# Performance work log

Hardware: AMD Instinct MI355X
Metric: run time of the kernel (lower is better)

## Reference

```python
import jax, jax.numpy as jnp
import numpy as np

STRIDE, PAD, DIL, DG, K = 1, 1, 1, 1, 3


def _conv2d(x, w, b, stride, pad):
    out = jax.lax.conv_general_dilated(
        x, w, (stride, stride), [(pad, pad), (pad, pad)],
        dimension_numbers=("NCHW", "OIHW", "NCHW"))
    return out + b[None, :, None, None]


def _deform_conv(x, weight, bias, offset, mask):
    # x: [B,C,H,W]; offset: [B, 2*DG*K*K, Ho, Wo] (y,x interleaved per tap);
    # mask: [B, DG*K*K, Ho, Wo]; weight: [Cout, C, K, K]
    B, C, H, W = x.shape
    Cout = weight.shape[0]
    KK = K * K
    Ho, Wo = offset.shape[2], offset.shape[3]
    Cg = C // DG

    off = offset.reshape(B, DG, KK, 2, Ho, Wo)
    dy, dx = off[:, :, :, 0], off[:, :, :, 1]          # [B,DG,KK,Ho,Wo]

    ky = (jnp.arange(KK) // K).astype(jnp.float32) * DIL
    kx = (jnp.arange(KK) % K).astype(jnp.float32) * DIL
    oy = (jnp.arange(Ho).astype(jnp.float32) * STRIDE - PAD)
    ox = (jnp.arange(Wo).astype(jnp.float32) * STRIDE - PAD)
    py = dy + ky[None, None, :, None, None] + oy[None, None, None, :, None]
    px = dx + kx[None, None, :, None, None] + ox[None, None, None, None, :]

    y0 = jnp.floor(py)
    x0 = jnp.floor(px)
    wy = py - y0
    wx = px - x0
    y0i = y0.astype(jnp.int32)
    x0i = x0.astype(jnp.int32)

    x_g = x.reshape(B, DG, Cg, H * W)
    val = jnp.zeros((B, DG, Cg, KK, Ho, Wo), dtype=x.dtype)
    corners = [(y0i, x0i, (1 - wy) * (1 - wx)),
               (y0i, x0i + 1, (1 - wy) * wx),
               (y0i + 1, x0i, wy * (1 - wx)),
               (y0i + 1, x0i + 1, wy * wx)]
    for iy, ix, wgt in corners:
        valid = ((iy >= 0) & (iy < H) & (ix >= 0) & (ix < W)).astype(x.dtype)
        idx = jnp.clip(iy, 0, H - 1) * W + jnp.clip(ix, 0, W - 1)  # [B,DG,KK,Ho,Wo]
        g = jnp.take_along_axis(x_g, idx.reshape(B, DG, 1, KK * Ho * Wo), axis=3)
        g = g.reshape(B, DG, Cg, KK, Ho, Wo)
        val = val + g * (wgt * valid)[:, :, None]

    m = mask.reshape(B, DG, 1, KK, Ho, Wo)
    val = (val * m).reshape(B, C, KK, Ho, Wo)
    out = jnp.einsum("bckhw,ock->bohw", val, weight.reshape(Cout, C, KK))
    return out + bias[None, :, None, None]


def setup_inputs() -> dict:
    key = jax.random.key(0)
    ks = jax.random.split(key, 5)
    B, C, H, W, Cout = 8, 64, 128, 128, 64
    x = jax.random.normal(ks[0], (B, C, H, W), dtype=jnp.float32)
    stdv = 1.0 / np.sqrt(C * K * K)
    weight = jax.random.uniform(ks[1], (Cout, C, K, K), minval=-stdv, maxval=stdv, dtype=jnp.float32)
    bias = jnp.zeros((Cout,), dtype=jnp.float32)
    # conv_offset params are zero-init in the original; use small random values
    offset_w = jax.random.normal(ks[2], (3 * DG * K * K, C, K, K), dtype=jnp.float32) * 0.01
    offset_b = jax.random.normal(ks[3], (3 * DG * K * K,), dtype=jnp.float32) * 0.01
    return {"x": x, "weight": weight, "bias": bias, "offset_w": offset_w, "offset_b": offset_b}


def reference(x, weight, bias, offset_w, offset_b):
    split = 2 * DG * K * K
    out = _conv2d(x, offset_w, offset_b, STRIDE, PAD)
    offset = out[:, :split]
    mask = jax.nn.sigmoid(out[:, split:])
    return _deform_conv(x, weight, bias, offset, mask)
```

## Files before the change

kernel.cpp:

```cpp
#include <hip/hip_runtime.h>
#include <hip/hip_bf16.h>
#include <math.h>

#define HH 128
#define WW 128
#define HW 16384
#define BATCH 8

#define TR 8
#define TC 16
#define HALO 2
#define PR 12
#define PC 20
#define PST 36

typedef __attribute__((ext_vector_type(8))) short short8;
typedef __attribute__((ext_vector_type(16))) float f32x16;
typedef __attribute__((ext_vector_type(4))) unsigned int u32x4;

union FragU { short8 v; unsigned int u[4]; u32x4 q; };

static __device__ __forceinline__ unsigned short f2bf(float f) {
    __hip_bfloat16 h = __float2bfloat16(f);
    return *(unsigned short*)&h;
}
static __device__ __forceinline__ float bf_lo(unsigned int r) {
    return __uint_as_float(r << 16);
}
static __device__ __forceinline__ float bf_hi(unsigned int r) {
    return __uint_as_float(r & 0xffff0000u);
}
static __device__ __forceinline__ short8 bilerp_frag(
    u32x4 r00, u32x4 r01, u32x4 r10, u32x4 r11,
    float w0, float w1, float w2, float w3)
{
    FragU bf;
#pragma unroll
    for (int d = 0; d < 4; ++d) {
        float se = fmaf(bf_lo(r11[d]), w3, fmaf(bf_lo(r10[d]), w2,
                   fmaf(bf_lo(r01[d]), w1, bf_lo(r00[d]) * w0)));
        float so = fmaf(bf_hi(r11[d]), w3, fmaf(bf_hi(r10[d]), w2,
                   fmaf(bf_hi(r01[d]), w1, bf_hi(r00[d]) * w0)));
        float2 f2; f2.x = se; f2.y = so;
        __hip_bfloat162 h2 = __float22bfloat162_rn(f2);
        bf.u[d] = *(unsigned int*)&h2;
    }
    return bf.v;
}

__global__ __launch_bounds__(256) void prep_kernel(
    const float* __restrict__ weight,
    const float* __restrict__ offset_w,
    unsigned short* __restrict__ wA,
    unsigned short* __restrict__ owA)
{
    int id = blockIdx.x * 256 + threadIdx.x;
    if (id < 4608) {
        int m = id / 2304;
        int rem = id % 2304;
        int kk = rem >> 8;
        int s = (rem >> 6) & 3;
        int l = id & 63;
        int cout = m * 32 + (l & 31);
        int cbase = s * 16 + 8 * (l >> 5);
#pragma unroll
        for (int j = 0; j < 8; ++j) {
            wA[id * 8 + j] = f2bf(weight[(cout * 64 + cbase + j) * 9 + kk]);
        }
        return;
    }
    int id2 = id - 4608;
    if (id2 < 2304) {
        int kk = id2 >> 8;
        int s = (id2 >> 6) & 3;
        int l = id2 & 63;
        int cout = l & 31;
        int cbase = s * 16 + 8 * (l >> 5);
#pragma unroll
        for (int j = 0; j < 8; ++j) {
            float v = (cout < 27) ? offset_w[(cout * 64 + cbase + j) * 9 + kk] : 0.0f;
            owA[id2 * 8 + j] = f2bf(v);
        }
    }
}

__global__ __launch_bounds__(256) void transform_kernel(
    const float* __restrict__ x,
    unsigned int* __restrict__ xT)
{
    __shared__ unsigned int lds[64][33];
    int bid = blockIdx.x;
    int b = bid & 7;
    int pix0 = (bid >> 3) << 6;
    int t = threadIdx.x;
    int px = t & 63;
    int cp0 = (t >> 6) * 8;

    const float* xb = x + (size_t)b * 64 * HW + pix0 + px;
#pragma unroll
    for (int it = 0; it < 8; ++it) {
        int cpair = cp0 + it;
        float2 f2;
        f2.x = xb[(size_t)(2 * cpair) * HW];
        f2.y = xb[(size_t)(2 * cpair + 1) * HW];
        __hip_bfloat162 h2 = __float22bfloat162_rn(f2);
        lds[px][cpair] = *(unsigned int*)&h2;
    }
    __syncthreads();

    int wpx = t >> 2, qq = t & 3;
    unsigned int* dst = xT + ((size_t)b * HW + pix0 + wpx) * 32 + qq * 8;
    u32x4 a, c;
#pragma unroll
    for (int j = 0; j < 4; ++j) a[j] = lds[wpx][qq * 8 + j];
#pragma unroll
    for (int j = 0; j < 4; ++j) c[j] = lds[wpx][qq * 8 + 4 + j];
    *(u32x4*)dst = a;
    *(u32x4*)(dst + 4) = c;
}

__global__ __launch_bounds__(256, 3) void fused_kernel(
    const unsigned int* __restrict__ xT,
    const unsigned short* __restrict__ wA,
    const unsigned short* __restrict__ owA,
    const float* __restrict__ bias,
    const float* __restrict__ offset_b,
    float* __restrict__ out)
{
    __shared__ unsigned int patch[PR * PC * PST];
    __shared__ float red[4][27][33];

    int t = threadIdx.x;
    int lane = t & 63;
    int wid = t >> 6;
    int bid = blockIdx.x;
    int b = bid & 7;
    int tile = bid >> 3;
    int ho0 = (tile >> 3) * TR;
    int wo0 = (tile & 7) * TC;
    int py0 = ho0 - HALO;
    int px0 = wo0 - HALO;

    int q = lane & 31;
    int hi = lane >> 5;
    int ho = ho0 + 2 * wid + (q >> 4);
    int wo = wo0 + (q & 15);
    int p = ho * WW + wo;

    const unsigned int* xb = xT + (size_t)b * HW * 32;
    const short8* wAv = (const short8*)wA;
    const short8* owAv = (const short8*)owA;

#pragma unroll
    for (int it = 0; it < 8; ++it) {
        int id = it * 256 + t;
        if (id < PR * PC * 8) {
            int row = id / (PC * 8);
            int rem = id - row * (PC * 8);
            int col = rem >> 3;
            int c = rem & 7;
            int yc = min(max(py0 + row, 0), HH - 1);
            int xc = min(max(px0 + col, 0), WW - 1);
            u32x4 v = *(const u32x4*)(xb + (size_t)(yc * WW + xc) * 32 + c * 4);
            *(u32x4*)&patch[(row * PC + col) * PST + c * 4] = v;
        }
    }
    __syncthreads();

    {
        f32x16 acc1 = {};
#pragma unroll
        for (int kk = 0; kk < 9; ++kk) {
            int iy = ho + kk / 3 - 1;
            int ix = wo + kk % 3 - 1;
            bool ok = ((unsigned)iy < 128u) && ((unsigned)ix < 128u);
            int jy = min(max(iy, 0), 127) - py0;
            int jx = min(max(ix, 0), 127) - px0;
            int base = (jy * PC + jx) * PST + (hi << 2);
#pragma unroll
            for (int s = 0; s < 4; ++s) {
                u32x4 raw = *(const u32x4*)&patch[base + s * 8];
                FragU bf;
#pragma unroll
                for (int j = 0; j < 4; ++j) bf.u[j] = ok ? raw[j] : 0u;
                acc1 = __builtin_amdgcn_mfma_f32_32x32x16_bf16(
                    owAv[(kk * 4 + s) * 64 + lane], bf.v, acc1, 0, 0, 0);
            }
        }
#pragma unroll
        for (int r = 0; r < 16; ++r) {
            int cout = (r & 3) + 8 * (r >> 2) + 4 * hi;
            if (cout < 27) {
                float a = acc1[r] + offset_b[cout];
                if (cout >= 18) a = 1.0f / (1.0f + __expf(-a));
                red[wid][cout][q] = a;
            }
        }
    }

    f32x16 acc[2];
#pragma unroll
    for (int m = 0; m < 2; ++m) {
#pragma unroll
        for (int r = 0; r < 16; ++r) {
            acc[m][r] = bias[m * 32 + (r & 3) + 8 * (r >> 2) + 4 * hi];
        }
    }

    for (int kk = 0; kk < 9; ++kk) {
        float dy = red[wid][2 * kk][q];
        float dx = red[wid][2 * kk + 1][q];
        float mm = red[wid][18 + kk][q];

        float py = dy + (float)(kk / 3 + ho - 1);
        float px = dx + (float)(kk % 3 + wo - 1);
        float y0f = floorf(py), x0f = floorf(px);
        float wy = py - y0f, wx = px - x0f;
        int y0 = (int)y0f, x0 = (int)x0f;
        int y1 = y0 + 1, x1 = x0 + 1;
        bool y0ok = (unsigned)y0 < 128u, y1ok = (unsigned)y1 < 128u;
        bool x0ok = (unsigned)x0 < 128u, x1ok = (unsigned)x1 < 128u;
        float w0 = (y0ok && x0ok) ? (1.0f - wy) * (1.0f - wx) * mm : 0.0f;
        float w1 = (y0ok && x1ok) ? (1.0f - wy) * wx * mm : 0.0f;
        float w2 = (y1ok && x0ok) ? wy * (1.0f - wx) * mm : 0.0f;
        float w3 = (y1ok && x1ok) ? wy * wx * mm : 0.0f;
        int y0c = min(max(y0, 0), 127), y1c = min(max(y1, 0), 127);
        int x0c = min(max(x0, 0), 127), x1c = min(max(x1, 0), 127);

        int jy0 = y0c - py0, jy1 = y1c - py0;
        int jx0 = x0c - px0, jx1 = x1c - px0;
        bool inp = ((unsigned)jy0 < (unsigned)PR) && ((unsigned)jy1 < (unsigned)PR) &&
                   ((unsigned)jx0 < (unsigned)PC) && ((unsigned)jx1 < (unsigned)PC);

#define P2_STEP(S, R00, R01, R10, R11) {                                    \
            short8 A0 = wAv[(kk * 4 + (S)) * 64 + lane];                    \
            short8 A1 = wAv[(36 + kk * 4 + (S)) * 64 + lane];               \
            short8 bf = bilerp_frag(R00, R01, R10, R11, w0, w1, w2, w3);    \
            acc[0] = __builtin_amdgcn_mfma_f32_32x32x16_bf16(A0, bf, acc[0], 0, 0, 0); \
            acc[1] = __builtin_amdgcn_mfma_f32_32x32x16_bf16(A1, bf, acc[1], 0, 0, 0); \
        }

        if (__all(inp)) {
            int b00 = (jy0 * PC + jx0) * PST + (hi << 2);
            int b01 = (jy0 * PC + jx1) * PST + (hi << 2);
            int b10 = (jy1 * PC + jx0) * PST + (hi << 2);
            int b11 = (jy1 * PC + jx1) * PST + (hi << 2);
#define LRD(B, S) (*(const u32x4*)&patch[(B) + (S) * 8])
            P2_STEP(0, LRD(b00,0), LRD(b01,0), LRD(b10,0), LRD(b11,0));
            P2_STEP(1, LRD(b00,1), LRD(b01,1), LRD(b10,1), LRD(b11,1));
            P2_STEP(2, LRD(b00,2), LRD(b01,2), LRD(b10,2), LRD(b11,2));
            P2_STEP(3, LRD(b00,3), LRD(b01,3), LRD(b10,3), LRD(b11,3));
#undef LRD
        } else {
            int o00 = (y0c * WW + x0c) * 32 + (hi << 2);
            int o01 = (y0c * WW + x1c) * 32 + (hi << 2);
            int o10 = (y1c * WW + x0c) * 32 + (hi << 2);
            int o11 = (y1c * WW + x1c) * 32 + (hi << 2);
#define GRD(O, S) (*(const u32x4*)(xb + (O) + (S) * 8))
            P2_STEP(0, GRD(o00,0), GRD(o01,0), GRD(o10,0), GRD(o11,0));
            P2_STEP(1, GRD(o00,1), GRD(o01,1), GRD(o10,1), GRD(o11,1));
            P2_STEP(2, GRD(o00,2), GRD(o01,2), GRD(o10,2), GRD(o11,2));
            P2_STEP(3, GRD(o00,3), GRD(o01,3), GRD(o10,3), GRD(o11,3));
#undef GRD
        }
#undef P2_STEP
    }

#pragma unroll
    for (int m = 0; m < 2; ++m) {
#pragma unroll
        for (int r = 0; r < 16; ++r) {
            int cout = m * 32 + (r & 3) + 8 * (r >> 2) + 4 * hi;
            out[((size_t)b * 64 + cout) * HW + p] = acc[m][r];
        }
    }
}

extern "C" void kernel_launch(void* const* d_in, const int* in_sizes, int n_in,
                              void* d_out, int out_size, void* d_ws, size_t ws_size,
                              hipStream_t stream) {
    const float* x        = (const float*)d_in[0];
    const float* weight   = (const float*)d_in[1];
    const float* bias     = (const float*)d_in[2];
    const float* offset_w = (const float*)d_in[3];
    const float* offset_b = (const float*)d_in[4];
    float* out = (float*)d_out;

    unsigned int* xT = (unsigned int*)d_ws;
    unsigned short* wA  = (unsigned short*)(xT + (size_t)BATCH * HW * 32);
    unsigned short* owA = wA + 4608 * 8;

    prep_kernel<<<27, 256, 0, stream>>>(weight, offset_w, wA, owA);

    int n_tiles = BATCH * HW / 64;
    transform_kernel<<<n_tiles, 256, 0, stream>>>(x, xT);

    int n_blocks = BATCH * HW / 128;
    fused_kernel<<<n_blocks, 256, 0, stream>>>(xT, wA, owA, bias, offset_b, out);
}
```

Measured before the change: 57.34 us.

## Replace LDS offset staging with cross-lane shuffles, packed bilerp math, raise occupancy

Measured after the change: 63.74 us. 11.2% more time.

```diff
diff --git a/kernel.cpp b/kernel.cpp
--- a/kernel.cpp
+++ b/kernel.cpp
@@ -17,6 +17,7 @@
 typedef __attribute__((ext_vector_type(8))) short short8;
 typedef __attribute__((ext_vector_type(16))) float f32x16;
 typedef __attribute__((ext_vector_type(4))) unsigned int u32x4;
+typedef __attribute__((ext_vector_type(2))) float f32x2;
 
 union FragU { short8 v; unsigned int u[4]; u32x4 q; };
 
@@ -24,29 +25,33 @@
     __hip_bfloat16 h = __float2bfloat16(f);
     return *(unsigned short*)&h;
 }
-static __device__ __forceinline__ float bf_lo(unsigned int r) {
-    return __uint_as_float(r << 16);
-}
-static __device__ __forceinline__ float bf_hi(unsigned int r) {
-    return __uint_as_float(r & 0xffff0000u);
+static __device__ __forceinline__ f32x2 upk2(unsigned int r) {
+    f32x2 v;
+    v.x = __uint_as_float(r << 16);
+    v.y = __uint_as_float(r & 0xffff0000u);
+    return v;
 }
 static __device__ __forceinline__ short8 bilerp_frag(
     u32x4 r00, u32x4 r01, u32x4 r10, u32x4 r11,
     float w0, float w1, float w2, float w3)
 {
     FragU bf;
+    f32x2 W0 = {w0, w0}, W1 = {w1, w1}, W2 = {w2, w2}, W3 = {w3, w3};
 #pragma unroll
     for (int d = 0; d < 4; ++d) {
-        float se = fmaf(bf_lo(r11[d]), w3, fmaf(bf_lo(r10[d]), w2,
-                   fmaf(bf_lo(r01[d]), w1, bf_lo(r00[d]) * w0)));
-        float so = fmaf(bf_hi(r11[d]), w3, fmaf(bf_hi(r10[d]), w2,
-                   fmaf(bf_hi(r01[d]), w1, bf_hi(r00[d]) * w0)));
-        float2 f2; f2.x = se; f2.y = so;
+        f32x2 s = upk2(r00[d]) * W0;
+        s = __builtin_elementwise_fma(upk2(r01[d]), W1, s);
+        s = __builtin_elementwise_fma(upk2(r10[d]), W2, s);
+        s = __builtin_elementwise_fma(upk2(r11[d]), W3, s);
+        float2 f2; f2.x = s.x; f2.y = s.y;
         __hip_bfloat162 h2 = __float22bfloat162_rn(f2);
         bf.u[d] = *(unsigned int*)&h2;
     }
     return bf.v;
 }
+
+#define RR(row) (((row) & 3) | (((row) >> 3) << 2))
+#define HB(row) ((((row) >> 2) & 1) << 5)
 
 __global__ __launch_bounds__(256) void prep_kernel(
     const float* __restrict__ weight,
@@ -119,7 +124,7 @@
     *(u32x4*)(dst + 4) = c;
 }
 
-__global__ __launch_bounds__(256, 3) void fused_kernel(
+__global__ __launch_bounds__(256, 4) void fused_kernel(
     const unsigned int* __restrict__ xT,
     const unsigned short* __restrict__ wA,
     const unsigned short* __restrict__ owA,
@@ -128,7 +133,6 @@
     float* __restrict__ out)
 {
     __shared__ unsigned int patch[PR * PC * PST];
-    __shared__ float red[4][27][33];
 
     int t = threadIdx.x;
     int lane = t & 63;
@@ -167,34 +171,32 @@
     }
     __syncthreads();
 
-    {
-        f32x16 acc1 = {};
-#pragma unroll
-        for (int kk = 0; kk < 9; ++kk) {
-            int iy = ho + kk / 3 - 1;
-            int ix = wo + kk % 3 - 1;
-            bool ok = ((unsigned)iy < 128u) && ((unsigned)ix < 128u);
-            int jy = min(max(iy, 0), 127) - py0;
-            int jx = min(max(ix, 0), 127) - px0;
-            int base = (jy * PC + jx) * PST + (hi << 2);
-#pragma unroll
-            for (int s = 0; s < 4; ++s) {
-                u32x4 raw = *(const u32x4*)&patch[base + s * 8];
-                FragU bf;
-#pragma unroll
-                for (int j = 0; j < 4; ++j) bf.u[j] = ok ? raw[j] : 0u;
-                acc1 = __builtin_amdgcn_mfma_f32_32x32x16_bf16(
-                    owAv[(kk * 4 + s) * 64 + lane], bf.v, acc1, 0, 0, 0);
-            }
-        }
-#pragma unroll
-        for (int r = 0; r < 16; ++r) {
-            int cout = (r & 3) + 8 * (r >> 2) + 4 * hi;
-            if (cout < 27) {
-                float a = acc1[r] + offset_b[cout];
-                if (cout >= 18) a = 1.0f / (1.0f + __expf(-a));
-                red[wid][cout][q] = a;
-            }
+    f32x16 acc1 = {};
+#pragma unroll
+    for (int kk = 0; kk < 9; ++kk) {
+        int iy = ho + kk / 3 - 1;
+        int ix = wo + kk % 3 - 1;
+        bool ok = ((unsigned)iy < 128u) && ((unsigned)ix < 128u);
+        int jy = min(max(iy, 0), 127) - py0;
+        int jx = min(max(ix, 0), 127) - px0;
+        int base = (jy * PC + jx) * PST + (hi << 2);
+#pragma unroll
+        for (int s = 0; s < 4; ++s) {
+            u32x4 raw = *(const u32x4*)&patch[base + s * 8];
+            FragU bf;
+#pragma unroll
+            for (int j = 0; j < 4; ++j) bf.u[j] = ok ? raw[j] : 0u;
+            acc1 = __builtin_amdgcn_mfma_f32_32x32x16_bf16(
+                owAv[(kk * 4 + s) * 64 + lane], bf.v, acc1, 0, 0, 0);
+        }
+    }
+#pragma unroll
+    for (int r = 0; r < 16; ++r) {
+        int cout = (r & 3) + 8 * (r >> 2) + 4 * hi;
+        if (cout < 27) {
+            float a = acc1[r] + offset_b[cout];
+            if (cout >= 18) a = 1.0f / (1.0f + __expf(-a));
+            acc1[r] = a;
         }
     }
 
@@ -207,10 +209,11 @@
         }
     }
 
+#pragma unroll
     for (int kk = 0; kk < 9; ++kk) {
-        float dy = red[wid][2 * kk][q];
-        float dx = red[wid][2 * kk + 1][q];
-        float mm = red[wid][18 + kk][q];
+        float dy = __shfl(acc1[RR(2 * kk)],     q + HB(2 * kk));
+        float dx = __shfl(acc1[RR(2 * kk + 1)], q + HB(2 * kk + 1));
+        float mm = __shfl(acc1[RR(18 + kk)],    q + HB(18 + kk));
 
         float py = dy + (float)(kk / 3 + ho - 1);
         float px = dx + (float)(kk % 3 + wo - 1);
```
